# Kernel optimization log

Measured on AMD Instinct MI355X. Metric: run time of the kernel, lower is better.

Reference implementation:

```python
import jax, jax.numpy as jnp
import numpy as np

B, S, ID = 4, 1024, 4096
R, RP, H, D = 512, 64, 32, 128  # lora_rank, rope_dim, n_heads, head_dim
EPS = 1.1920929e-07  # torch nn.RMSNorm default eps = finfo(float32).eps


def rms_norm(x, w):
    return x * jax.lax.rsqrt(jnp.mean(x * x, axis=-1, keepdims=True) + EPS) * w


def rope(x, cos_half, sin_half):
    # half/half pairing rotation (HF style)
    cos = jnp.concatenate([cos_half, cos_half], axis=-1)
    sin = jnp.concatenate([sin_half, sin_half], axis=-1)
    half = x.shape[-1] // 2
    rot = jnp.concatenate([-x[..., half:], x[..., :half]], axis=-1)
    return x * cos + rot * sin


def setup_inputs() -> dict:
    key = jax.random.key(0)
    ks = jax.random.split(key, 12)
    sc = 0.02
    x = jax.random.normal(ks[0], (B, S, ID), jnp.float32)
    # real RoPE tables, shape (S, RP//2)
    inv_freq = 1.0 / (10000.0 ** (jnp.arange(0, RP, 2, dtype=jnp.float32) / RP))
    ang = jnp.arange(S, dtype=jnp.float32)[:, None] * inv_freq[None, :]
    cos_half = jnp.cos(ang)
    sin_half = jnp.sin(ang)
    mask = jnp.zeros((S, S), jnp.float32)  # additive mask; no softmax in module so keep finite
    return {
        "x": x,
        "cos_half": cos_half,
        "sin_half": sin_half,
        "mask": mask,
        "w_dkv_kr_w": jax.random.normal(ks[1], (R + RP, ID), jnp.float32) * sc,
        "w_dkv_kr_b": jnp.zeros((R + RP,), jnp.float32),
        "kv_norm_w": jnp.ones((R,), jnp.float32),
        "w_dq_w": jax.random.normal(ks[2], (R, ID), jnp.float32) * sc,
        "w_dq_b": jnp.zeros((R,), jnp.float32),
        "q_norm_w": jnp.ones((R,), jnp.float32),
        "w_uq_w": jax.random.normal(ks[3], (H * D, R), jnp.float32) * sc,
        "w_uq_b": jnp.zeros((H * D,), jnp.float32),
        "w_qr_w": jax.random.normal(ks[4], (RP, R), jnp.float32) * sc,
        "w_qr_b": jnp.zeros((RP,), jnp.float32),
        "w_uk_w": jax.random.normal(ks[5], (H * D, R), jnp.float32) * sc,
        "w_uv_w": jax.random.normal(ks[6], (H * D, R), jnp.float32) * sc,
        "w_o_w": jax.random.normal(ks[7], (ID, H * D), jnp.float32) * sc,
        "w_o_b": jnp.zeros((ID,), jnp.float32),
        "start_pos": 0,
    }


def reference(x, cos_half, sin_half, mask, w_dkv_kr_w, w_dkv_kr_b, kv_norm_w,
              w_dq_w, w_dq_b, q_norm_w, w_uq_w, w_uq_b, w_qr_w, w_qr_b,
              w_uk_w, w_uv_w, w_o_w, w_o_b, start_pos):
    b, s, _ = x.shape
    # KV down-projection + decoupled rope key
    dkv = x @ w_dkv_kr_w.T + w_dkv_kr_b                      # (b,s,R+RP)
    c_kv = rms_norm(dkv[..., :R], kv_norm_w)                 # (b,s,R) == kv_cache[:,start:end] (start_pos=0, prefill)
    k_r = rope(dkv[..., R:], cos_half, sin_half)             # (b,s,RP) == pe_cache slice
    # Q path
    c_q = rms_norm(x @ w_dq_w.T + w_dq_b, q_norm_w)          # (b,s,R)
    q = (c_q @ w_uq_w.T + w_uq_b).reshape(b, s, H, D)        # (b,s,h,d)
    q_r = rope(c_q @ w_qr_w.T + w_qr_b, cos_half, sin_half)  # (b,s,RP)
    # weight absorption: fold w_uk into the query
    qW = jnp.einsum('bshd,hdr->bshr', q, w_uk_w.reshape(H, D, R))
    scores = jnp.einsum('bshr,btr->bsht', qW, c_kv)
    scores = scores + jnp.einsum('bsd,btd->bst', q_r, k_r)[:, :, None, :]
    scores = scores + mask[:, None, :]                       # (s,1,t) broadcast over (b,s,h,t)
    # NOTE: faithful to source -- no softmax / no scaling applied
    a_sum = jnp.einsum('bsht,btr->bshr', scores, c_kv)
    out = jnp.einsum('bshr,hdr->bshd', a_sum, w_uv_w.reshape(H, D, R))
    out = out.reshape(b, s, H * D)
    return out @ w_o_w.T + w_o_b
```

## Files before the change

kernel.cpp:

```cpp
#include <hip/hip_runtime.h>
#include <hip/hip_bf16.h>

typedef __attribute__((ext_vector_type(8))) short s8v;
typedef __attribute__((ext_vector_type(4))) float f4v;
typedef __hip_bfloat16 bf16;

#define BSZ 4
#define SEQ 1024
#define IDIM 4096
#define RNK 512
#define RPD 64
#define NH 32
#define HD 128
#define BT 4096

__device__ __forceinline__ void load_lds16(const bf16* g, bf16* l) {
  __builtin_amdgcn_global_load_lds((const __attribute__((address_space(1))) void*)g,
                                   (__attribute__((address_space(3))) void*)l, 16, 0, 0);
}

template<int OUT_BF16, int HAS_BIAS>
__global__ __launch_bounds__(256, 2) void gemmT(
    const bf16* __restrict__ A, const bf16* __restrict__ B, void* __restrict__ Cv,
    const float* __restrict__ bias, int K, int lda, int ldb, int ldc, int NYT)
{
  __shared__ bf16 As[2][128 * 32];
  __shared__ bf16 Bs[2][256 * 32];

  int nwg = gridDim.x, orig = blockIdx.x, cpx = nwg >> 3;
  int lin = (orig & 7) * cpx + (orig >> 3);
  int ty = lin % NYT, tx = lin / NYT;
  long long rowBase = (long long)ty * 128;
  long long colBase = (long long)tx * 256;

  int tid = threadIdx.x, lane = tid & 63, wave = tid >> 6;
  int wr = wave >> 1, wc = wave & 1;
  int NT = K >> 5;

  const bf16* aSrc[2]; int aDst[2];
  #pragma unroll
  for (int j = 0; j < 2; ++j) {
    int c = j * 256 + tid, r = c >> 2, sp = c & 3, s = sp ^ ((r >> 1) & 3);
    aSrc[j] = A + (rowBase + r) * lda + s * 8;
    aDst[j] = c * 8;
  }
  const bf16* bSrc[4]; int bDst[4];
  #pragma unroll
  for (int j = 0; j < 4; ++j) {
    int c = j * 256 + tid, r = c >> 2, sp = c & 3, s = sp ^ ((r >> 1) & 3);
    bSrc[j] = B + (colBase + r) * ldb + s * 8;
    bDst[j] = c * 8;
  }

#define STAGE(bs, kt) do {                                                    \
    _Pragma("unroll")                                                         \
    for (int j_ = 0; j_ < 2; ++j_)                                            \
      load_lds16(aSrc[j_] + (long long)(kt) * 32, &As[bs][aDst[j_]]);         \
    _Pragma("unroll")                                                         \
    for (int j_ = 0; j_ < 4; ++j_)                                            \
      load_lds16(bSrc[j_] + (long long)(kt) * 32, &Bs[bs][bDst[j_]]);         \
  } while (0)

  int aOff[4], bOff[8];
  #pragma unroll
  for (int f = 0; f < 4; ++f) {
    int row = wr * 64 + f * 16 + (lane & 15);
    aOff[f] = row * 32 + (((lane >> 4) ^ ((row >> 1) & 3)) * 8);
  }
  #pragma unroll
  for (int f = 0; f < 8; ++f) {
    int row = wc * 128 + f * 16 + (lane & 15);
    bOff[f] = row * 32 + (((lane >> 4) ^ ((row >> 1) & 3)) * 8);
  }

  f4v acc[4][8];
  #pragma unroll
  for (int m = 0; m < 4; ++m)
    #pragma unroll
    for (int n = 0; n < 8; ++n) acc[m][n] = {0.f, 0.f, 0.f, 0.f};

#define COMPUTE(bs) do {                                                      \
    s8v av[4], bv[8];                                                         \
    _Pragma("unroll")                                                         \
    for (int f_ = 0; f_ < 4; ++f_) av[f_] = *(const s8v*)&As[bs][aOff[f_]];   \
    _Pragma("unroll")                                                         \
    for (int f_ = 0; f_ < 8; ++f_) bv[f_] = *(const s8v*)&Bs[bs][bOff[f_]];   \
    _Pragma("unroll")                                                         \
    for (int m_ = 0; m_ < 4; ++m_)                                            \
      _Pragma("unroll")                                                       \
      for (int n_ = 0; n_ < 8; ++n_)                                          \
        acc[m_][n_] = __builtin_amdgcn_mfma_f32_16x16x32_bf16(                \
            av[m_], bv[n_], acc[m_][n_], 0, 0, 0);                            \
  } while (0)

  STAGE(0, 0);
  for (int u = 0; u < NT; u += 2) {
    __syncthreads();
    if (u + 1 < NT) STAGE(1, u + 1);
    COMPUTE(0);
    __syncthreads();
    if (u + 2 < NT) STAGE(0, u + 2);
    COMPUTE(1);
  }
#undef STAGE
#undef COMPUTE

  float* Cf = (float*)Cv;
  bf16* Cb = (bf16*)Cv;
  int lcol = lane & 15, lr4 = (lane >> 4) * 4;
  #pragma unroll
  for (int m = 0; m < 4; ++m)
    #pragma unroll
    for (int n = 0; n < 8; ++n) {
      long long col = colBase + wc * 128 + n * 16 + lcol;
      float bv_ = HAS_BIAS ? bias[col] : 0.f;
      #pragma unroll
      for (int j = 0; j < 4; ++j) {
        long long row = rowBase + wr * 64 + m * 16 + lr4 + j;
        float v = acc[m][n][j] + bv_;
        if (OUT_BF16) Cb[row * ldc + col] = __float2bfloat16(v);
        else          Cf[row * ldc + col] = v;
      }
    }
}

template<int BM, int BN, int WTM, int WTN, int OUT_BF16, int ADD_MODE, int HAS_BIAS>
__global__ __launch_bounds__(256) void gemm_bt(
    const bf16* __restrict__ A, const bf16* __restrict__ B, void* __restrict__ Cv,
    const float* __restrict__ bias, const void* __restrict__ addend,
    int K, int lda, int ldb, int ldc, int ldadd, int nz2,
    long long sA1, long long sA2, long long sB1, long long sB2,
    long long sC1, long long sC2, long long sD1, long long sD2)
{
  constexpr int BK = 32;
  constexpr int WM = BM / WTM, WN = BN / WTN;
  constexpr int FM = WM / 16, FN = WN / 16;
  static_assert(WTM * WTN == 4, "4 waves / 256 threads");
  static_assert((BM * BK) % 2048 == 0 && (BN * BK) % 2048 == 0, "staging coverage");
  __shared__ alignas(16) bf16 As[BM * BK];
  __shared__ alignas(16) bf16 Bs[BN * BK];

  int z = blockIdx.z;
  int z1 = z / nz2, z2 = z - z1 * nz2;
  A += z1 * sA1 + z2 * sA2;
  B += z1 * sB1 + z2 * sB2;
  long long coff = z1 * sC1 + z2 * sC2;
  long long doffz = z1 * sD1 + z2 * sD2;

  int tid = threadIdx.x;
  int lane = tid & 63, wave = tid >> 6;
  int wr = wave / WTN, wc = wave % WTN;
  int rowBase = blockIdx.y * BM;
  int colBase = blockIdx.x * BN;

  f4v acc[FM][FN];
  #pragma unroll
  for (int i = 0; i < FM; ++i)
    #pragma unroll
    for (int j = 0; j < FN; ++j) acc[i][j] = {0.f, 0.f, 0.f, 0.f};

  constexpr int A_LOADS = (BM * BK) / 2048;
  constexpr int B_LOADS = (BN * BK) / 2048;
  int lrow = lane & 15, lk = (lane >> 4) * 8;

  for (int k0 = 0; k0 < K; k0 += BK) {
    #pragma unroll
    for (int i = 0; i < A_LOADS; ++i) {
      int e = tid * 8 + i * 2048;
      load_lds16(A + (long long)(rowBase + (e >> 5)) * lda + k0 + (e & 31), &As[e]);
    }
    #pragma unroll
    for (int i = 0; i < B_LOADS; ++i) {
      int e = tid * 8 + i * 2048;
      load_lds16(B + (long long)(colBase + (e >> 5)) * ldb + k0 + (e & 31), &Bs[e]);
    }
    __syncthreads();

    s8v av[FM], bv[FN];
    #pragma unroll
    for (int fm = 0; fm < FM; ++fm)
      av[fm] = *(const s8v*)&As[(wr * WM + fm * 16 + lrow) * BK + lk];
    #pragma unroll
    for (int fn = 0; fn < FN; ++fn)
      bv[fn] = *(const s8v*)&Bs[(wc * WN + fn * 16 + lrow) * BK + lk];
    #pragma unroll
    for (int fm = 0; fm < FM; ++fm)
      #pragma unroll
      for (int fn = 0; fn < FN; ++fn)
        acc[fm][fn] = __builtin_amdgcn_mfma_f32_16x16x32_bf16(av[fm], bv[fn], acc[fm][fn], 0, 0, 0);
    __syncthreads();
  }

  bf16* Cb = (bf16*)Cv;
  float* Cf = (float*)Cv;
  const float* addf = (const float*)addend;
  const bf16* addb = (const bf16*)addend;
  int lcol = lane & 15, lr4 = (lane >> 4) * 4;
  #pragma unroll
  for (int fm = 0; fm < FM; ++fm) {
    #pragma unroll
    for (int fn = 0; fn < FN; ++fn) {
      int col = colBase + wc * WN + fn * 16 + lcol;
      #pragma unroll
      for (int j = 0; j < 4; ++j) {
        int row = rowBase + wr * WM + fm * 16 + lr4 + j;
        float v = acc[fm][fn][j];
        if (HAS_BIAS) v += bias[col];
        if (ADD_MODE == 1) v += addf[doffz + (long long)row * ldadd + col];
        if (ADD_MODE == 2) v += __bfloat162float(addb[doffz + (long long)row * ldadd + col]);
        long long idx = coff + (long long)row * ldc + col;
        if (OUT_BF16) Cb[idx] = __float2bfloat16(v);
        else          Cf[idx] = v;
      }
    }
  }
}


__global__ void cast4(const float* __restrict__ in, bf16* __restrict__ out, int n4) {
  int i = blockIdx.x * 256 + threadIdx.x;
  if (i >= n4) return;
  float4 v = ((const float4*)in)[i];
  union { ushort4 u; bf16 h[4]; } o;
  o.h[0] = __float2bfloat16(v.x); o.h[1] = __float2bfloat16(v.y);
  o.h[2] = __float2bfloat16(v.z); o.h[3] = __float2bfloat16(v.w);
  ((ushort4*)out)[i] = o.u;
}

struct CastJobs {
  const float* s[8];
  bf16* d[8];
  int n4[8];
  int b0[8];
};
__global__ __launch_bounds__(256) void cast_multi(CastJobs J) {
  int blk = blockIdx.x, j = 0;
  #pragma unroll
  for (int k = 1; k < 8; ++k) if (blk >= J.b0[k]) j = k;
  int i = (blk - J.b0[j]) * 256 + threadIdx.x;
  if (i >= J.n4[j]) return;
  float4 v = ((const float4*)J.s[j])[i];
  union { ushort4 u; bf16 h[4]; } o;
  o.h[0] = __float2bfloat16(v.x); o.h[1] = __float2bfloat16(v.y);
  o.h[2] = __float2bfloat16(v.z); o.h[3] = __float2bfloat16(v.w);
  ((ushort4*)J.d[j])[i] = o.u;
}

__global__ __launch_bounds__(256) void tr_bf16(const bf16* __restrict__ in, bf16* __restrict__ out,
                                               int R, int C) {
  __shared__ bf16 t[32][33];
  long long zo = (long long)blockIdx.z * R * C;
  int c0 = blockIdx.x * 32, r0 = blockIdx.y * 32;
  int tx = threadIdx.x & 31, ty = threadIdx.x >> 5;
  #pragma unroll
  for (int i = 0; i < 32; i += 8)
    t[ty + i][tx] = in[zo + (long long)(r0 + ty + i) * C + (c0 + tx)];
  __syncthreads();
  #pragma unroll
  for (int i = 0; i < 32; i += 8)
    out[zo + (long long)(c0 + ty + i) * R + (r0 + tx)] = t[tx][ty + i];
}

__device__ __forceinline__ float block_sum256(float v) {
  #pragma unroll
  for (int o = 32; o > 0; o >>= 1) v += __shfl_xor(v, o, 64);
  __shared__ float red[4];
  int lane = threadIdx.x & 63, w = threadIdx.x >> 6;
  if (lane == 0) red[w] = v;
  __syncthreads();
  return red[0] + red[1] + red[2] + red[3];
}

__global__ __launch_bounds__(256) void rms_dkv(const float* __restrict__ dq,
    const float* __restrict__ w, const float* __restrict__ ch, const float* __restrict__ sh,
    bf16* __restrict__ ckv, bf16* __restrict__ kr) {
  int row = blockIdx.x, t = threadIdx.x;
  const float* xr = dq + (long long)row * 1088;
  float v0 = xr[t], v1 = xr[t + 256];
  float ss = block_sum256(v0 * v0 + v1 * v1);
  float sc = rsqrtf(ss * (1.0f / 512.0f) + 1.1920929e-07f);
  long long o = (long long)row * 512;
  ckv[o + t]       = __float2bfloat16(v0 * sc * w[t]);
  ckv[o + t + 256] = __float2bfloat16(v1 * sc * w[t + 256]);
  if (t < 64) {
    int s = row & (SEQ - 1);
    float a = xr[512 + t], r;
    if (t < 32) r = a * ch[s * 32 + t]      - xr[512 + t + 32] * sh[s * 32 + t];
    else        r = a * ch[s * 32 + t - 32] + xr[512 + t - 32] * sh[s * 32 + t - 32];
    kr[(long long)row * 64 + t] = __float2bfloat16(r);
  }
}

__global__ __launch_bounds__(256) void rms512(const float* __restrict__ dq,
    const float* __restrict__ w, bf16* __restrict__ out) {
  int row = blockIdx.x, t = threadIdx.x;
  const float* xr = dq + (long long)row * 1088 + 576;
  float v0 = xr[t], v1 = xr[t + 256];
  float ss = block_sum256(v0 * v0 + v1 * v1);
  float sc = rsqrtf(ss * (1.0f / 512.0f) + 1.1920929e-07f);
  long long o = (long long)row * 512;
  out[o + t]       = __float2bfloat16(v0 * sc * w[t]);
  out[o + t + 256] = __float2bfloat16(v1 * sc * w[t + 256]);
}

__global__ void rope_qr(const float* __restrict__ in, const float* __restrict__ ch,
                        const float* __restrict__ sh, bf16* __restrict__ out) {
  int row = blockIdx.x, t = threadIdx.x;
  const float* xr = in + (long long)row * 64;
  int s = row & (SEQ - 1);
  float a = xr[t], r;
  if (t < 32) r = a * ch[s * 32 + t]      - xr[t + 32] * sh[s * 32 + t];
  else        r = a * ch[s * 32 + t - 32] + xr[t - 32] * sh[s * 32 + t - 32];
  out[(long long)row * 64 + t] = __float2bfloat16(r);
}

extern "C" void kernel_launch(void* const* d_in, const int* in_sizes, int n_in,
                              void* d_out, int out_size, void* d_ws, size_t ws_size,
                              hipStream_t stream) {
  const float* x    = (const float*)d_in[0];
  const float* ch   = (const float*)d_in[1];
  const float* sh   = (const float*)d_in[2];
  const float* mask = (const float*)d_in[3];
  const float* wdkv = (const float*)d_in[4];
  const float* bdkv = (const float*)d_in[5];
  const float* kvnw = (const float*)d_in[6];
  const float* wdq  = (const float*)d_in[7];
  const float* bdq  = (const float*)d_in[8];
  const float* qnw  = (const float*)d_in[9];
  const float* wuq  = (const float*)d_in[10];
  const float* buq  = (const float*)d_in[11];
  const float* wqr  = (const float*)d_in[12];
  const float* bqr  = (const float*)d_in[13];
  const float* wuk  = (const float*)d_in[14];
  const float* wuv  = (const float*)d_in[15];
  const float* wo   = (const float*)d_in[16];
  const float* bo   = (const float*)d_in[17];
  float* out = (float*)d_out;
  (void)in_sizes; (void)n_in; (void)out_size; (void)ws_size;

  char* ws = (char*)d_ws;
  bf16* regionA = (bf16*)(ws);
  bf16* outh    = (bf16*)(ws + 33554432);
  bf16* wdkv_b  = (bf16*)(ws + 67108864);
  bf16* wdq_b   = (bf16*)(ws + 71827456);
  bf16* wuq_b   = (bf16*)(ws + 76021760);
  bf16* wqr_b   = (bf16*)(ws + 80216064);
  bf16* wuv_b   = (bf16*)(ws + 80281600);
  bf16* wuk_b   = (bf16*)(ws + 84475904);
  bf16* mask_b  = (bf16*)(ws + 88670208);
  char* regionB = ws + 90767360;
  float* dq_cat = (float*)(regionB);
  bf16* Eb      = (bf16*)(regionB);
  bf16* FT      = (bf16*)(regionB + 16777216);

  bf16* xb   = regionA;
  bf16* wo_b = regionA;

  char* ob = (char*)d_out;
  bf16* qb     = (bf16*)(ob);
  char* U      = ob + 33554432;
  bf16* ckv    = (bf16*)(U);
  bf16* kr     = (bf16*)(U + 4194304);
  bf16* ckvT   = (bf16*)(U + 4718592);
  bf16* krT    = (bf16*)(U + 8912896);
  bf16* cq     = (bf16*)(U + 9437184);
  float* qr_pre= (float*)(U + 13631488);
  bf16* qr_b   = (bf16*)(U + 14680064);
  bf16* Gm     = (bf16*)(U + 15204352);
  bf16* Mt     = (bf16*)(U + 17301504);
  bf16* base_b = (bf16*)(U + 17563648);

  float* bias_cat = qr_pre;

  long long Z = 0;

  {
    CastJobs J;
    const float* srcs[8] = {x, wdkv, wdq, wqr, mask, wuq, wuv, wuk};
    bf16* dsts[8] = {xb, wdkv_b, wdq_b, wqr_b, mask_b, wuq_b, wuv_b, wuk_b};
    int n4s[8] = {4194304, 589824, 524288, 8192, 262144, 524288, 524288, 524288};
    int accb = 0;
    for (int j = 0; j < 8; ++j) {
      J.s[j] = srcs[j]; J.d[j] = dsts[j]; J.n4[j] = n4s[j];
      J.b0[j] = accb; accb += (n4s[j] + 255) / 256;
    }
    cast_multi<<<dim3(accb), 256, 0, stream>>>(J);
  }
  hipMemcpyAsync(bias_cat, bdkv, 576 * 4, hipMemcpyDeviceToDevice, stream);
  hipMemcpyAsync(bias_cat + 576, bdq, 512 * 4, hipMemcpyDeviceToDevice, stream);

  gemm_bt<128, 64, 4, 1, 0, 0, 1><<<dim3(17, 32, 1), 256, 0, stream>>>(
      xb, wdkv_b, dq_cat, bias_cat, nullptr, 4096, 4096, 4096, 1088, 0, 1, Z,Z,Z,Z,Z,Z,Z,Z);
  rms_dkv<<<dim3(BT), 256, 0, stream>>>(dq_cat, kvnw, ch, sh, ckv, kr);
  rms512<<<dim3(BT), 256, 0, stream>>>(dq_cat, qnw, cq);
  tr_bf16<<<dim3(16, 32, 4), 256, 0, stream>>>(ckv, ckvT, 1024, 512);
  tr_bf16<<<dim3(2, 32, 4), 256, 0, stream>>>(kr, krT, 1024, 64);

  cast4<<<dim3(16384), 256, 0, stream>>>(wo, wo_b, 4194304);

  gemmT<1, 1><<<dim3(512), 256, 0, stream>>>(
      cq, wuq_b, qb, buq, 512, 512, 512, 4096, 32);

  gemm_bt<128, 64, 4, 1, 0, 0, 1><<<dim3(1, 32, 1), 256, 0, stream>>>(
      cq, wqr_b, qr_pre, bqr, nullptr, 512, 512, 512, 64, 0, 1, Z,Z,Z,Z,Z,Z,Z,Z);
  rope_qr<<<dim3(BT), 64, 0, stream>>>(qr_pre, ch, sh, qr_b);

  gemm_bt<128, 128, 2, 2, 1, 0, 0><<<dim3(4, 4, 4), 256, 0, stream>>>(
      ckvT, ckvT, Gm, nullptr, nullptr, 1024, 1024, 1024, 512, 0, 1,
      524288LL, Z, 524288LL, Z, 262144LL, Z, Z, Z);

  gemm_bt<128, 64, 4, 1, 1, 0, 0><<<dim3(1, 4, 4), 256, 0, stream>>>(
      ckvT, krT, Mt, nullptr, nullptr, 1024, 1024, 1024, 64, 0, 1,
      524288LL, Z, 65536LL, Z, 32768LL, Z, Z, Z);

  gemm_bt<128, 128, 2, 2, 1, 0, 0><<<dim3(4, 8, 4), 256, 0, stream>>>(
      mask_b, ckvT, base_b, nullptr, nullptr, 1024, 1024, 1024, 512, 0, 1,
      Z, Z, 524288LL, Z, 524288LL, Z, Z, Z);

  gemm_bt<128, 128, 2, 2, 1, 2, 0><<<dim3(4, 8, 4), 256, 0, stream>>>(
      qr_b, Mt, base_b, nullptr, base_b, 64, 64, 64, 512, 512, 1,
      65536LL, Z, 32768LL, Z, 524288LL, Z, 524288LL, Z);

  gemmT<1, 0><<<dim3(512), 256, 0, stream>>>(
      base_b, wuv_b, outh, nullptr, 512, 512, 512, 4096, 32);

  gemm_bt<128, 128, 2, 2, 1, 0, 0><<<dim3(4, 1, 128), 256, 0, stream>>>(
      wuv_b, Gm, Eb, nullptr, nullptr, 512, 512, 512, 512, 0, 32,
      Z, 65536LL, 262144LL, Z, 2097152LL, 65536LL, Z, Z);

  gemm_bt<128, 128, 2, 2, 1, 0, 0><<<dim3(1, 1, 128), 256, 0, stream>>>(
      Eb, wuk_b, FT, nullptr, nullptr, 512, 512, 512, 128, 0, 32,
      2097152LL, 65536LL, Z, 65536LL, 524288LL, 16384LL, Z, Z);

  gemm_bt<128, 128, 2, 2, 1, 2, 0><<<dim3(1, 8, 128), 256, 0, stream>>>(
      qb, FT, outh, nullptr, outh, 128, 4096, 128, 4096, 4096, 32,
      4194304LL, 128LL, 524288LL, 16384LL, 4194304LL, 128LL, 4194304LL, 128LL);

  gemmT<0, 1><<<dim3(512), 256, 0, stream>>>(
      outh, wo_b, out, bo, 4096, 4096, 4096, 4096, 32);
}
```

Before: 485.5 us.

## Replace big GEMM kernel with 256x256 tile, 8-wave, phased pipelined kernel

Replaces the 128x256-tile GEMM with a 256x256-tile, BK=64, 512-thread kernel. The new kernel splits each K tile into four phases that interleave global-to-LDS loads with MFMA work, using explicit waitcnt/barrier control and setprio. The goal is to overlap memory traffic with compute and raise arithmetic intensity on the large projections (w_uq, w_uv, w_o). Separately, the generic gemm_bt gains an XOR swizzle on its LDS layout to cut bank conflicts. In exchange it uses more LDS and registers, has fewer workgroups per launch, and relies on fragile hand-written synchronisation.

```diff
diff --git a/kernel.cpp b/kernel.cpp
--- a/kernel.cpp
+++ b/kernel.cpp
@@ -20,103 +20,121 @@
 }
 
 template<int OUT_BF16, int HAS_BIAS>
-__global__ __launch_bounds__(256, 2) void gemmT(
+__global__ __launch_bounds__(512, 2) void gemm256(
     const bf16* __restrict__ A, const bf16* __restrict__ B, void* __restrict__ Cv,
-    const float* __restrict__ bias, int K, int lda, int ldb, int ldc, int NYT)
+    const float* __restrict__ bias, int K, int lda, int ldb, int ldc, int NXT)
 {
-  __shared__ bf16 As[2][128 * 32];
-  __shared__ bf16 Bs[2][256 * 32];
+  __shared__ bf16 As[2][256 * 64];
+  __shared__ bf16 Bs[2][256 * 64];
 
   int nwg = gridDim.x, orig = blockIdx.x, cpx = nwg >> 3;
-  int lin = (orig & 7) * cpx + (orig >> 3);
-  int ty = lin % NYT, tx = lin / NYT;
-  long long rowBase = (long long)ty * 128;
+  int l = (orig & 7) * cpx + (orig >> 3);
+  int tx = l % NXT, ty = l / NXT;
+  long long rowBase = (long long)ty * 256;
   long long colBase = (long long)tx * 256;
 
   int tid = threadIdx.x, lane = tid & 63, wave = tid >> 6;
-  int wr = wave >> 1, wc = wave & 1;
-  int NT = K >> 5;
-
-  const bf16* aSrc[2]; int aDst[2];
-  #pragma unroll
-  for (int j = 0; j < 2; ++j) {
-    int c = j * 256 + tid, r = c >> 2, sp = c & 3, s = sp ^ ((r >> 1) & 3);
-    aSrc[j] = A + (rowBase + r) * lda + s * 8;
-    aDst[j] = c * 8;
+  int wr = wave >> 2, wc = wave & 3;
+  int lrow = lane & 15, lslot = lane >> 4;
+  int NT = K >> 6;
+
+  int srow = tid >> 3, sslot = tid & 7;
+  int skc = sslot ^ (srow & 7);
+  const bf16* aS = A + (rowBase + srow) * lda + (skc << 3);
+  const bf16* bS = B + (colBase + srow) * ldb + (skc << 3);
+  int sdst = srow * 64 + sslot * 8;
+
+#define SG_A(bs, kt, roff) load_lds16(aS + (long long)(roff) * lda + ((long long)(kt) << 6), \
+                                      &As[bs][sdst + (roff) * 64])
+#define SG_B(bs, kt, roff) load_lds16(bS + (long long)(roff) * ldb + ((long long)(kt) << 6), \
+                                      &Bs[bs][sdst + (roff) * 64])
+
+  int offk0 = ((lslot ^ (lrow & 7)) << 3);
+  int offk1 = (((4 | lslot) ^ (lrow & 7)) << 3);
+  int aoff = (wr * 128 + lrow) * 64;
+  int boff = (wc * 64 + lrow) * 64;
+
+  f4v acc[8][4];
+  #pragma unroll
+  for (int m = 0; m < 8; ++m)
+    #pragma unroll
+    for (int n = 0; n < 4; ++n) acc[m][n] = {0.f, 0.f, 0.f, 0.f};
+
+#define PHASE(BSEL, Q, STG, GATE) do {                                         \
+    const bf16* Ab_ = &As[BSEL][aoff];                                         \
+    s8v a00 = *(const s8v*)(Ab_ + (2*(Q))   * 1024 + offk0);                   \
+    s8v a01 = *(const s8v*)(Ab_ + (2*(Q))   * 1024 + offk1);                   \
+    s8v a10 = *(const s8v*)(Ab_ + (2*(Q)+1) * 1024 + offk0);                   \
+    s8v a11 = *(const s8v*)(Ab_ + (2*(Q)+1) * 1024 + offk1);                   \
+    if ((Q) == 0) {                                                            \
+      const bf16* Bb_ = &Bs[BSEL][boff];                                       \
+      _Pragma("unroll")                                                        \
+      for (int n = 0; n < 4; ++n) {                                            \
+        b0[n] = *(const s8v*)(Bb_ + n * 1024 + offk0);                         \
+        b1[n] = *(const s8v*)(Bb_ + n * 1024 + offk1);                         \
+      }                                                                        \
+    }                                                                          \
+    STG;                                                                       \
+    if ((Q) == 0) asm volatile("s_waitcnt lgkmcnt(8)" ::: "memory");           \
+    asm volatile("s_barrier" ::: "memory");                                    \
+    asm volatile("s_waitcnt lgkmcnt(0)" ::: "memory");                         \
+    __builtin_amdgcn_sched_barrier(0);                                         \
+    __builtin_amdgcn_s_setprio(1);                                             \
+    _Pragma("unroll")                                                          \
+    for (int n = 0; n < 4; ++n)                                                \
+      acc[2*(Q)][n]   = __builtin_amdgcn_mfma_f32_16x16x32_bf16(a00, b0[n], acc[2*(Q)][n], 0, 0, 0);   \
+    _Pragma("unroll")                                                          \
+    for (int n = 0; n < 4; ++n)                                                \
+      acc[2*(Q)+1][n] = __builtin_amdgcn_mfma_f32_16x16x32_bf16(a10, b0[n], acc[2*(Q)+1][n], 0, 0, 0); \
+    _Pragma("unroll")                                                          \
+    for (int n = 0; n < 4; ++n)                                                \
+      acc[2*(Q)][n]   = __builtin_amdgcn_mfma_f32_16x16x32_bf16(a01, b1[n], acc[2*(Q)][n], 0, 0, 0);   \
+    _Pragma("unroll")                                                          \
+    for (int n = 0; n < 4; ++n)                                                \
+      acc[2*(Q)+1][n] = __builtin_amdgcn_mfma_f32_16x16x32_bf16(a11, b1[n], acc[2*(Q)+1][n], 0, 0, 0); \
+    __builtin_amdgcn_s_setprio(0);                                             \
+    GATE;                                                                      \
+    asm volatile("s_barrier" ::: "memory");                                    \
+  } while (0)
+
+  SG_B(0, 0, 0); SG_B(0, 0, 64); SG_B(0, 0, 128); SG_B(0, 0, 192);
+  SG_A(0, 0, 0); SG_A(0, 0, 64); SG_A(0, 0, 128); SG_A(0, 0, 192);
+  SG_B(1, 1, 0); SG_B(1, 1, 64); SG_B(1, 1, 128); SG_B(1, 1, 192);
+  SG_A(1, 1, 0); SG_A(1, 1, 128);
+  asm volatile("s_waitcnt vmcnt(6)" ::: "memory");
+  asm volatile("s_barrier" ::: "memory");
+
+  for (int u = 0; u < NT; u += 2) {
+    bool st2 = (u + 2 < NT);
+    s8v b0[4], b1[4];
+    PHASE(0, 0, { SG_A(1, u + 1, 64); SG_A(1, u + 1, 192); }, {});
+    PHASE(0, 1, { if (st2) { SG_B(0, u + 2, 0);   SG_B(0, u + 2, 64);  } }, {});
+    PHASE(0, 2, { if (st2) { SG_B(0, u + 2, 128); SG_B(0, u + 2, 192); } }, {});
+    PHASE(0, 3, { if (st2) { SG_A(0, u + 2, 0);   SG_A(0, u + 2, 128); } },
+          { if (st2) asm volatile("s_waitcnt vmcnt(6)" ::: "memory");
+            else     asm volatile("s_waitcnt vmcnt(0)" ::: "memory"); });
+    PHASE(1, 0, { if (st2) { SG_A(0, u + 2, 64);  SG_A(0, u + 2, 192); } }, {});
+    PHASE(1, 1, { if (st2) { SG_B(1, u + 3, 0);   SG_B(1, u + 3, 64);  } }, {});
+    PHASE(1, 2, { if (st2) { SG_B(1, u + 3, 128); SG_B(1, u + 3, 192); } }, {});
+    PHASE(1, 3, { if (st2) { SG_A(1, u + 3, 0);   SG_A(1, u + 3, 128); } },
+          { if (st2) asm volatile("s_waitcnt vmcnt(6)" ::: "memory"); });
   }
-  const bf16* bSrc[4]; int bDst[4];
-  #pragma unroll
-  for (int j = 0; j < 4; ++j) {
-    int c = j * 256 + tid, r = c >> 2, sp = c & 3, s = sp ^ ((r >> 1) & 3);
-    bSrc[j] = B + (colBase + r) * ldb + s * 8;
-    bDst[j] = c * 8;
-  }
-
-#define STAGE(bs, kt) do {                                                    \
-    _Pragma("unroll")                                                         \
-    for (int j_ = 0; j_ < 2; ++j_)                                            \
-      load_lds16(aSrc[j_] + (long long)(kt) * 32, &As[bs][aDst[j_]]);         \
-    _Pragma("unroll")                                                         \
-    for (int j_ = 0; j_ < 4; ++j_)                                            \
-      load_lds16(bSrc[j_] + (long long)(kt) * 32, &Bs[bs][bDst[j_]]);         \
-  } while (0)
-
-  int aOff[4], bOff[8];
-  #pragma unroll
-  for (int f = 0; f < 4; ++f) {
-    int row = wr * 64 + f * 16 + (lane & 15);
-    aOff[f] = row * 32 + (((lane >> 4) ^ ((row >> 1) & 3)) * 8);
-  }
-  #pragma unroll
-  for (int f = 0; f < 8; ++f) {
-    int row = wc * 128 + f * 16 + (lane & 15);
-    bOff[f] = row * 32 + (((lane >> 4) ^ ((row >> 1) & 3)) * 8);
-  }
-
-  f4v acc[4][8];
-  #pragma unroll
-  for (int m = 0; m < 4; ++m)
-    #pragma unroll
-    for (int n = 0; n < 8; ++n) acc[m][n] = {0.f, 0.f, 0.f, 0.f};
-
-#define COMPUTE(bs) do {                                                      \
-    s8v av[4], bv[8];                                                         \
-    _Pragma("unroll")                                                         \
-    for (int f_ = 0; f_ < 4; ++f_) av[f_] = *(const s8v*)&As[bs][aOff[f_]];   \
-    _Pragma("unroll")                                                         \
-    for (int f_ = 0; f_ < 8; ++f_) bv[f_] = *(const s8v*)&Bs[bs][bOff[f_]];   \
-    _Pragma("unroll")                                                         \
-    for (int m_ = 0; m_ < 4; ++m_)                                            \
-      _Pragma("unroll")                                                       \
-      for (int n_ = 0; n_ < 8; ++n_)                                          \
-        acc[m_][n_] = __builtin_amdgcn_mfma_f32_16x16x32_bf16(                \
-            av[m_], bv[n_], acc[m_][n_], 0, 0, 0);                            \
-  } while (0)
-
-  STAGE(0, 0);
-  for (int u = 0; u < NT; u += 2) {
-    __syncthreads();
-    if (u + 1 < NT) STAGE(1, u + 1);
-    COMPUTE(0);
-    __syncthreads();
-    if (u + 2 < NT) STAGE(0, u + 2);
-    COMPUTE(1);
-  }
-#undef STAGE
-#undef COMPUTE
+#undef PHASE
+#undef SG_A
+#undef SG_B
 
   float* Cf = (float*)Cv;
   bf16* Cb = (bf16*)Cv;
   int lcol = lane & 15, lr4 = (lane >> 4) * 4;
   #pragma unroll
-  for (int m = 0; m < 4; ++m)
-    #pragma unroll
-    for (int n = 0; n < 8; ++n) {
-      long long col = colBase + wc * 128 + n * 16 + lcol;
+  for (int m = 0; m < 8; ++m)
+    #pragma unroll
+    for (int n = 0; n < 4; ++n) {
+      long long col = colBase + wc * 64 + n * 16 + lcol;
       float bv_ = HAS_BIAS ? bias[col] : 0.f;
       #pragma unroll
       for (int j = 0; j < 4; ++j) {
-        long long row = rowBase + wr * 64 + m * 16 + lr4 + j;
+        long long row = rowBase + wr * 128 + m * 16 + lr4 + j;
         float v = acc[m][n][j] + bv_;
         if (OUT_BF16) Cb[row * ldc + col] = __float2bfloat16(v);
         else          Cf[row * ldc + col] = v;
@@ -161,28 +179,32 @@
 
   constexpr int A_LOADS = (BM * BK) / 2048;
   constexpr int B_LOADS = (BN * BK) / 2048;
-  int lrow = lane & 15, lk = (lane >> 4) * 8;
+  int lrow = lane & 15;
+  int rsw = (lrow >> 1) & 3;
+  int lkA = ((lane >> 4) ^ rsw) * 8;
 
   for (int k0 = 0; k0 < K; k0 += BK) {
     #pragma unroll
     for (int i = 0; i < A_LOADS; ++i) {
       int e = tid * 8 + i * 2048;
-      load_lds16(A + (long long)(rowBase + (e >> 5)) * lda + k0 + (e & 31), &As[e]);
+      int r_ = e >> 5, sp_ = (e >> 3) & 3, kc_ = sp_ ^ ((r_ >> 1) & 3);
+      load_lds16(A + (long long)(rowBase + r_) * lda + k0 + (kc_ << 3), &As[e]);
     }
     #pragma unroll
     for (int i = 0; i < B_LOADS; ++i) {
       int e = tid * 8 + i * 2048;
-      load_lds16(B + (long long)(colBase + (e >> 5)) * ldb + k0 + (e & 31), &Bs[e]);
+      int r_ = e >> 5, sp_ = (e >> 3) & 3, kc_ = sp_ ^ ((r_ >> 1) & 3);
+      load_lds16(B + (long long)(colBase + r_) * ldb + k0 + (kc_ << 3), &Bs[e]);
     }
     __syncthreads();
 
     s8v av[FM], bv[FN];
     #pragma unroll
     for (int fm = 0; fm < FM; ++fm)
-      av[fm] = *(const s8v*)&As[(wr * WM + fm * 16 + lrow) * BK + lk];
+      av[fm] = *(const s8v*)&As[(wr * WM + fm * 16 + lrow) * BK + lkA];
     #pragma unroll
     for (int fn = 0; fn < FN; ++fn)
-      bv[fn] = *(const s8v*)&Bs[(wc * WN + fn * 16 + lrow) * BK + lk];
+      bv[fn] = *(const s8v*)&Bs[(wc * WN + fn * 16 + lrow) * BK + lkA];
     #pragma unroll
     for (int fm = 0; fm < FM; ++fm)
       #pragma unroll
@@ -398,8 +420,8 @@
 
   cast4<<<dim3(16384), 256, 0, stream>>>(wo, wo_b, 4194304);
 
-  gemmT<1, 1><<<dim3(512), 256, 0, stream>>>(
-      cq, wuq_b, qb, buq, 512, 512, 512, 4096, 32);
+  gemm256<1, 1><<<dim3(256), 512, 0, stream>>>(
+      cq, wuq_b, qb, buq, 512, 512, 512, 4096, 16);
 
   gemm_bt<128, 64, 4, 1, 0, 0, 1><<<dim3(1, 32, 1), 256, 0, stream>>>(
       cq, wqr_b, qr_pre, bqr, nullptr, 512, 512, 512, 64, 0, 1, Z,Z,Z,Z,Z,Z,Z,Z);
@@ -421,8 +443,8 @@
       qr_b, Mt, base_b, nullptr, base_b, 64, 64, 64, 512, 512, 1,
       65536LL, Z, 32768LL, Z, 524288LL, Z, 524288LL, Z);
 
-  gemmT<1, 0><<<dim3(512), 256, 0, stream>>>(
-      base_b, wuv_b, outh, nullptr, 512, 512, 512, 4096, 32);
+  gemm256<1, 0><<<dim3(256), 512, 0, stream>>>(
+      base_b, wuv_b, outh, nullptr, 512, 512, 512, 4096, 16);
 
   gemm_bt<128, 128, 2, 2, 1, 0, 0><<<dim3(4, 1, 128), 256, 0, stream>>>(
       wuv_b, Gm, Eb, nullptr, nullptr, 512, 512, 512, 512, 0, 32,
@@ -436,6 +458,6 @@
       qb, FT, outh, nullptr, outh, 128, 4096, 128, 4096, 4096, 32,
       4194304LL, 128LL, 524288LL, 16384LL, 4194304LL, 128LL, 4194304LL, 128LL);
 
-  gemmT<0, 1><<<dim3(512), 256, 0, stream>>>(
-      outh, wo_b, out, bo, 4096, 4096, 4096, 4096, 32);
-}
+  gemm256<0, 1><<<dim3(256), 512, 0, stream>>>(
+      outh, wo_b, out, bo, 4096, 4096, 4096, 4096, 16);
+}
```

After: 459.6 us. -5.3%, faster.
